# Kernel optimization log

Measured on AMD Instinct MI355X. Metric: run time of the kernel, lower is better.

## Reference

```python
import jax, jax.numpy as jnp
import numpy as np

B, T, E, H = 2, 2048, 1024, 4
Dk = E // H          # 256 head qk dim
Dv = Dk * 2          # 512 head v dim (expansion_ratio=2)
EPS = 1e-5
ROPE_BASE = 10000.0


def setup_inputs() -> dict:
    key = jax.random.key(0)
    ks = jax.random.split(key, 7)
    s = 0.02  # small init matching xavier gains in reset_parameters
    return {
        "x": jax.random.normal(ks[0], (B, T, E), jnp.float32),
        "Wq": jax.random.normal(ks[1], (E, E), jnp.float32) * s,
        "Wk": jax.random.normal(ks[2], (E, E), jnp.float32) * s,
        "Wv": jax.random.normal(ks[3], (E, 2 * E), jnp.float32) * s,
        "Wg": jax.random.normal(ks[4], (E, 2 * E), jnp.float32) * s,
        "Wo": jax.random.normal(ks[5], (2 * E, E), jnp.float32) * s,
        "gn_weight": jnp.ones((Dv,), jnp.float32),
    }


def _rotary(q, k):
    # q,k: [b, t, h, d]; non-interleaved (GPT-NeoX) rotary over the full head dim
    d = q.shape[-1]
    inv_freq = 1.0 / (ROPE_BASE ** (jnp.arange(0, d, 2, dtype=jnp.float32) / d))
    t = jnp.arange(q.shape[1], dtype=jnp.float32)
    freqs = jnp.einsum('t,f->tf', t, inv_freq)      # [t, d/2]
    cos = jnp.cos(freqs)[None, :, None, :]
    sin = jnp.sin(freqs)[None, :, None, :]

    def rot(x):
        x1, x2 = x[..., : d // 2], x[..., d // 2:]
        return jnp.concatenate([x1 * cos - x2 * sin, x2 * cos + x1 * sin], axis=-1)

    return rot(q), rot(k)


def reference(x, Wq, Wk, Wv, Wg, Wo, gn_weight):
    b, t, e = x.shape
    q = (x @ Wq).reshape(b, t, H, Dk)
    k = (x @ Wk).reshape(b, t, H, Dk)
    q, k = _rotary(q, k)
    q = q.transpose(0, 2, 1, 3) * (Dk ** -0.5)      # [b,h,t,dk], scale = head_qk_dim^-0.5
    k = k.transpose(0, 2, 1, 3)
    v = (x @ Wv).reshape(b, t, H, Dv).transpose(0, 2, 1, 3)  # [b,h,t,dv]

    # RetNet per-head decay: gamma_h = 1 - 2^-(5+h)
    gamma = 1.0 - jnp.exp2(-5.0 - jnp.arange(H, dtype=jnp.float32))
    ti = jnp.arange(t)
    n = ti[:, None] - ti[None, :]                   # t - s
    decay = jnp.where(
        n >= 0,
        gamma[:, None, None] ** jnp.maximum(n, 0).astype(jnp.float32),
        0.0,
    )                                               # [h,t,t] causal decayed mask

    scores = jnp.einsum('bhtd,bhsd->bhts', q, k) * decay[None]
    o = jnp.einsum('bhts,bhsd->bhtd', scores, v)    # [b,h,t,dv]
    o = o.transpose(0, 2, 1, 3)                     # [b,t,h,dv]

    # per-head RMSNorm (group_norm over head_v_dim)
    rms = jnp.sqrt(jnp.mean(o * o, axis=-1, keepdims=True) + EPS)
    o = o / rms * gn_weight

    # NOTE: the given source multiplies by raw g_proj(x) (gate_fn not applied in forward)
    g = x @ Wg                                      # [b,t,2E]
    return (o.reshape(b, t, H * Dv) * g) @ Wo       # [b,t,E]
```

## Files before the change

### kernel.cpp

```cpp
#include <hip/hip_runtime.h>
#include <hip/hip_bf16.h>

#define B_ 2
#define T_ 2048
#define E_ 1024
#define DK 256
#define DV 512
#define MROWS 4096
#define LDQKVG 6144
#define LDOG 2048

typedef __attribute__((ext_vector_type(8))) short short8;
typedef __attribute__((ext_vector_type(4))) float floatx4;

typedef __attribute__((address_space(3))) unsigned as3_u32;
typedef const __attribute__((address_space(1))) unsigned as1_u32;

static __device__ __forceinline__ void gld_lds16(const unsigned short* gsrc, unsigned short* ldst) {
  __builtin_amdgcn_global_load_lds((as1_u32*)gsrc, (as3_u32*)ldst, 16, 0, 0);
}

static __device__ __forceinline__ float bf2f(unsigned short u) {
  union { unsigned int i; float f; } x; x.i = ((unsigned int)u) << 16; return x.f;
}
static __device__ __forceinline__ unsigned short f2bf(float f) {
  __hip_bfloat16 h = __float2bfloat16(f);
  return __builtin_bit_cast(unsigned short, h);
}
static __device__ __forceinline__ float load_as_f(const float* p) { return *p; }
static __device__ __forceinline__ float load_as_f(const unsigned short* p) { return bf2f(*p); }

__global__ void __launch_bounds__(256) convx_kernel(const float* __restrict__ x,
                                                    unsigned short* __restrict__ xb) {
  int i = blockIdx.x * 256 + threadIdx.x;
  size_t base = (size_t)i * 8;
  float4 a = *(const float4*)(x + base);
  float4 b = *(const float4*)(x + base + 4);
  short8 o;
  o[0] = (short)f2bf(a.x); o[1] = (short)f2bf(a.y);
  o[2] = (short)f2bf(a.z); o[3] = (short)f2bf(a.w);
  o[4] = (short)f2bf(b.x); o[5] = (short)f2bf(b.y);
  o[6] = (short)f2bf(b.z); o[7] = (short)f2bf(b.w);
  *(short8*)(xb + base) = o;
}

template<typename TIN>
__global__ void __launch_bounds__(256) transpose_bf16_kernel(
    const TIN* __restrict__ in, int ldin, unsigned short* __restrict__ out, int ldout) {
  __shared__ float tile[32][33];
  int c0 = blockIdx.x * 32, r0 = blockIdx.y * 32;
  int tx = threadIdx.x & 31, ty = threadIdx.x >> 5;
#pragma unroll
  for (int i = 0; i < 32; i += 8)
    tile[ty + i][tx] = load_as_f(&in[(size_t)(r0 + ty + i) * ldin + c0 + tx]);
  __syncthreads();
#pragma unroll
  for (int i = 0; i < 32; i += 8)
    out[(size_t)(c0 + ty + i) * ldout + r0 + tx] = f2bf(tile[tx][ty + i]);
}

template<int MTILE, bool F32OUT>
__global__ void __launch_bounds__(256) gemm_bt_kernel(
    const unsigned short* __restrict__ A, const unsigned short* __restrict__ Bt,
    void* __restrict__ Cp, int K, int ldc, int ccol0) {
  __shared__ unsigned short As[MTILE * 32];
  __shared__ unsigned short Bs[128 * 32];
  constexpr int MB = MTILE / 32;
  constexpr int AJ = MTILE / 64;
  const int tid = threadIdx.x;
  const int lane = tid & 63;
  const int wid = tid >> 6;
  const int m0 = blockIdx.x * MTILE;
  const int n0 = blockIdx.y * 128;
  const int wr = (wid >> 1) * (MTILE / 2), wc = (wid & 1) * 64;
  floatx4 acc[MB][4];
#pragma unroll
  for (int i = 0; i < MB; i++)
#pragma unroll
    for (int j = 0; j < 4; j++)
      acc[i][j] = (floatx4){0.f, 0.f, 0.f, 0.f};

  for (int k0 = 0; k0 < K; k0 += 32) {
    __syncthreads();
#pragma unroll
    for (int j = 0; j < AJ; ++j) {
      int ci = (wid * AJ + j) * 64 + lane;
      int row = ci >> 2, cc = (ci & 3) * 8;
      gld_lds16(&A[(size_t)(m0 + row) * K + k0 + cc], &As[(wid * AJ + j) * 512]);
    }
#pragma unroll
    for (int j = 0; j < 2; ++j) {
      int ci = (wid * 2 + j) * 64 + lane;
      int row = ci >> 2, cc = (ci & 3) * 8;
      gld_lds16(&Bt[(size_t)(n0 + row) * K + k0 + cc], &Bs[(wid * 2 + j) * 512]);
    }
    __syncthreads();
    short8 af[MB], bfr[4];
#pragma unroll
    for (int mb = 0; mb < MB; mb++)
      af[mb] = *(const short8*)&As[(wr + mb * 16 + (lane & 15)) * 32 + (lane >> 4) * 8];
#pragma unroll
    for (int nb = 0; nb < 4; nb++)
      bfr[nb] = *(const short8*)&Bs[(wc + nb * 16 + (lane & 15)) * 32 + (lane >> 4) * 8];
#pragma unroll
    for (int mb = 0; mb < MB; mb++)
#pragma unroll
      for (int nb = 0; nb < 4; nb++)
        acc[mb][nb] = __builtin_amdgcn_mfma_f32_16x16x32_bf16(af[mb], bfr[nb], acc[mb][nb], 0, 0, 0);
  }
#pragma unroll
  for (int mb = 0; mb < MB; mb++)
#pragma unroll
    for (int nb = 0; nb < 4; nb++)
#pragma unroll
      for (int r = 0; r < 4; r++) {
        int row = m0 + wr + mb * 16 + (lane >> 4) * 4 + r;
        int col = ccol0 + n0 + wc + nb * 16 + (lane & 15);
        float v = acc[mb][nb][r];
        if (F32OUT) ((float*)Cp)[(size_t)row * ldc + col] = v;
        else ((unsigned short*)Cp)[(size_t)row * ldc + col] = f2bf(v);
      }
}

__global__ void __launch_bounds__(256) rope_kernel(unsigned short* __restrict__ qkvg) {
  int idx = blockIdx.x * 256 + threadIdx.x;
  int j = idx & 127;
  int h = (idx >> 7) & 3;
  int row = idx >> 9;
  int t = row & (T_ - 1);
  float invf = exp2f(-(float)j * (13.287712379549449f / 128.0f));
  float ang = (float)t * invf;
  float c = cosf(ang), s = sinf(ang);
  size_t base = (size_t)row * LDQKVG + h * DK + j;
  float q1 = bf2f(qkvg[base]), q2 = bf2f(qkvg[base + 128]);
  float k1 = bf2f(qkvg[base + E_]), k2 = bf2f(qkvg[base + E_ + 128]);
  qkvg[base]            = f2bf((q1 * c - q2 * s) * 0.0625f);
  qkvg[base + 128]      = f2bf((q2 * c + q1 * s) * 0.0625f);
  qkvg[base + E_]       = f2bf(k1 * c - k2 * s);
  qkvg[base + E_ + 128] = f2bf(k2 * c + k1 * s);
}

__global__ void __launch_bounds__(256) retention_kernel(
    const unsigned short* __restrict__ qkvg, const unsigned short* __restrict__ vT,
    const float* __restrict__ gnw, unsigned short* __restrict__ og,
    float* __restrict__ ssbuf) {
  __shared__ unsigned short k_lds[2][32 * 256];
  __shared__ unsigned short v_lds[2][256 * 32];
  __shared__ unsigned short s_lds[2][16 * 40];
  __shared__ float rms_lds[32][2];
  const int tid = threadIdx.x, lane = tid & 63, wid = tid >> 6;
  const int rh = wid & 1, dh = wid >> 1;
  const int bh = blockIdx.x & 7, dvh = (blockIdx.x >> 3) & 1, p = blockIdx.x >> 4;
  const int b = bh >> 2, h = bh & 3;
  const float log2g = log2f(1.0f - exp2f(-5.0f - (float)h));
  const unsigned short* kbase = qkvg + (size_t)b * T_ * LDQKVG + E_ + h * DK;
  const unsigned short* vbase = vT + (size_t)(h * DV + dvh * 256) * MROWS + b * T_;

  auto stage = [&](int buf, int sb) {
    int s0 = sb * 32;
#pragma unroll
    for (int j = 0; j < 4; ++j) {
      int ci = (wid * 4 + j) * 64 + lane;
      int row = ci >> 5, c = ci & 31;
      int cs = c ^ (row & 7);
      gld_lds16(kbase + (size_t)(s0 + row) * LDQKVG + cs * 8, &k_lds[buf][(wid * 4 + j) * 512]);
    }
#pragma unroll
    for (int j = 0; j < 4; ++j) {
      int ci = (wid * 4 + j) * 64 + lane;
      int dv = ci >> 2, c = ci & 3;
      int cs = c ^ ((dv ^ (dv >> 2)) & 3);
      gld_lds16(vbase + (size_t)dv * MROWS + s0 + cs * 8, &v_lds[buf][(wid * 4 + j) * 512]);
    }
  };

#pragma unroll 1
  for (int half = 0; half < 2; ++half) {
    const int tt = half == 0 ? p : 63 - p;
    const int r0 = tt * 32;
    const int nsb = tt + 1;

    short8 qf[8];
    {
      int qrow = b * T_ + r0 + rh * 16 + (lane & 15);
      const unsigned short* qp = qkvg + (size_t)qrow * LDQKVG + h * DK + (lane >> 4) * 8;
#pragma unroll
      for (int kk = 0; kk < 8; kk++) qf[kk] = *(const short8*)(qp + kk * 32);
    }
    floatx4 oacc[8];
#pragma unroll
    for (int i = 0; i < 8; i++) oacc[i] = (floatx4){0.f, 0.f, 0.f, 0.f};

    stage(0, 0);
#pragma unroll 1
    for (int sb = 0; sb < nsb; ++sb) {
      const int cur = sb & 1;
      __syncthreads();
      floatx4 f = (floatx4){0.f, 0.f, 0.f, 0.f};
      const int scol_l = dh * 16 + (lane & 15);
#pragma unroll
      for (int kk = 0; kk < 8; kk++) {
        int c = (kk * 4 + (lane >> 4)) ^ (scol_l & 7);
        short8 kf = *(const short8*)&k_lds[cur][scol_l * 256 + c * 8];
        f = __builtin_amdgcn_mfma_f32_16x16x32_bf16(qf[kk], kf, f, 0, 0, 0);
      }
      const int s0 = sb * 32;
#pragma unroll
      for (int r = 0; r < 4; ++r) {
        int lr = (lane >> 4) * 4 + r;
        int qrow_h = r0 + rh * 16 + lr;
        int scol = s0 + dh * 16 + (lane & 15);
        int n = qrow_h - scol;
        float val = (n >= 0) ? f[r] * exp2f((float)n * log2g) : 0.0f;
        s_lds[rh][lr * 40 + dh * 16 + (lane & 15)] = f2bf(val);
      }
      __syncthreads();
      if (sb + 1 < nsb) stage(cur ^ 1, sb + 1);
      short8 af = *(const short8*)&s_lds[rh][(lane & 15) * 40 + (lane >> 4) * 8];
#pragma unroll
      for (int nb = 0; nb < 8; ++nb) {
        int dv = dh * 128 + nb * 16 + (lane & 15);
        int c = (lane >> 4) ^ ((dv ^ (dv >> 2)) & 3);
        short8 vf = *(const short8*)&v_lds[cur][dv * 32 + c * 8];
        oacc[nb] = __builtin_amdgcn_mfma_f32_16x16x32_bf16(af, vf, oacc[nb], 0, 0, 0);
      }
    }
#pragma unroll
    for (int r = 0; r < 4; ++r) {
      float ss = 0.f;
#pragma unroll
      for (int nb = 0; nb < 8; nb++) { float xv = oacc[nb][r]; ss += xv * xv; }
      ss += __shfl_xor(ss, 1, 64);
      ss += __shfl_xor(ss, 2, 64);
      ss += __shfl_xor(ss, 4, 64);
      ss += __shfl_xor(ss, 8, 64);
      if ((lane & 15) == 0) rms_lds[rh * 16 + (lane >> 4) * 4 + r][dh] = ss;
    }
    __syncthreads();
    if (dh == 0 && (lane & 15) == 0) {
#pragma unroll
      for (int r = 0; r < 4; ++r) {
        int rl = rh * 16 + (lane >> 4) * 4 + r;
        ssbuf[(size_t)(b * T_ + r0 + rl) * 8 + h * 2 + dvh] = rms_lds[rl][0] + rms_lds[rl][1];
      }
    }
#pragma unroll
    for (int r = 0; r < 4; ++r) {
      int rl = rh * 16 + (lane >> 4) * 4 + r;
      int qrow = b * T_ + r0 + rl;
      size_t growbase = (size_t)qrow * LDQKVG + 4096 + h * DV + dvh * 256 + dh * 128;
      size_t orowbase = (size_t)qrow * LDOG + h * DV + dvh * 256 + dh * 128;
#pragma unroll
      for (int nb = 0; nb < 8; nb++) {
        int col = nb * 16 + (lane & 15);
        float gv = bf2f(qkvg[growbase + col]);
        og[orowbase + col] = f2bf(oacc[nb][r] * gnw[dvh * 256 + dh * 128 + col] * gv);
      }
    }
    __syncthreads();
  }
}

__global__ void __launch_bounds__(256) normalize_kernel(
    unsigned short* __restrict__ og, const float* __restrict__ ssbuf) {
  int i = blockIdx.x * 256 + threadIdx.x;
  size_t e0 = (size_t)i * 8;
  int row = (int)(e0 >> 11);
  int col = (int)(e0 & 2047);
  int h = col >> 9;
  float ss = ssbuf[(size_t)row * 8 + h * 2] + ssbuf[(size_t)row * 8 + h * 2 + 1];
  float inv = rsqrtf(ss * (1.0f / 512.0f) + 1e-5f);
  short8 v = *(const short8*)(og + e0);
#pragma unroll
  for (int j = 0; j < 8; j++) v[j] = (short)f2bf(bf2f((unsigned short)v[j]) * inv);
  *(short8*)(og + e0) = v;
}

extern "C" void kernel_launch(void* const* d_in, const int* in_sizes, int n_in,
                              void* d_out, int out_size, void* d_ws, size_t ws_size,
                              hipStream_t stream) {
  const float* x   = (const float*)d_in[0];
  const float* Wq  = (const float*)d_in[1];
  const float* Wk  = (const float*)d_in[2];
  const float* Wv  = (const float*)d_in[3];
  const float* Wg  = (const float*)d_in[4];
  const float* Wo  = (const float*)d_in[5];
  const float* gnw = (const float*)d_in[6];
  float* out = (float*)d_out;

  char* ws = (char*)d_ws;
  size_t off = 0;
  auto alloc = [&](size_t bytes) { char* p = ws + off; off += (bytes + 255) & ~(size_t)255; return p; };
  unsigned short* xb    = (unsigned short*)alloc((size_t)MROWS * E_ * 2);
  unsigned short* WallT = (unsigned short*)alloc((size_t)6144 * 1024 * 2);
  unsigned short* WoT   = (unsigned short*)alloc((size_t)1024 * 2048 * 2);
  unsigned short* qkvg  = (unsigned short*)alloc((size_t)MROWS * LDQKVG * 2);
  unsigned short* vT    = (unsigned short*)alloc((size_t)2048 * MROWS * 2);
  unsigned short* og    = (unsigned short*)alloc((size_t)MROWS * LDOG * 2);
  float*          ssbuf = (float*)alloc((size_t)MROWS * 8 * 4);

  convx_kernel<<<2048, 256, 0, stream>>>(x, xb);

  transpose_bf16_kernel<float><<<dim3(32, 32), 256, 0, stream>>>(Wq, 1024, WallT, 1024);
  transpose_bf16_kernel<float><<<dim3(32, 32), 256, 0, stream>>>(Wk, 1024, WallT + (size_t)1024 * 1024, 1024);
  transpose_bf16_kernel<float><<<dim3(64, 32), 256, 0, stream>>>(Wv, 2048, WallT + (size_t)2048 * 1024, 1024);
  transpose_bf16_kernel<float><<<dim3(64, 32), 256, 0, stream>>>(Wg, 2048, WallT + (size_t)4096 * 1024, 1024);
  transpose_bf16_kernel<float><<<dim3(32, 64), 256, 0, stream>>>(Wo, 1024, WoT, 2048);

  gemm_bt_kernel<128, false><<<dim3(32, 48), 256, 0, stream>>>(xb, WallT, qkvg, 1024, LDQKVG, 0);

  rope_kernel<<<8192, 256, 0, stream>>>(qkvg);

  transpose_bf16_kernel<unsigned short><<<dim3(64, 128), 256, 0, stream>>>(qkvg + 2048, LDQKVG, vT, MROWS);

  retention_kernel<<<512, 256, 0, stream>>>(qkvg, vT, gnw, og, ssbuf);

  normalize_kernel<<<4096, 256, 0, stream>>>(og, ssbuf);

  gemm_bt_kernel<64, true><<<dim3(64, 8), 256, 0, stream>>>(og, WoT, out, 2048, E_, 0);
}
```

Before: 240.7 us.

## Switch retention to chunkwise form with inter-chunk recurrent state

```diff
diff --git a/kernel.cpp b/kernel.cpp
--- a/kernel.cpp
+++ b/kernel.cpp
@@ -8,9 +8,11 @@
 #define DV 512
 #define MROWS 4096
 #define LDQKVG 6144
-#define LDOG 2048
+#define CHK 128
+#define NCHK 16
 
 typedef __attribute__((ext_vector_type(8))) short short8;
+typedef __attribute__((ext_vector_type(4))) short short4v;
 typedef __attribute__((ext_vector_type(4))) float floatx4;
 
 typedef __attribute__((address_space(3))) unsigned as3_u32;
@@ -59,10 +61,29 @@
     out[(size_t)(c0 + ty + i) * ldout + r0 + tx] = f2bf(tile[tx][ty + i]);
 }
 
+__global__ void __launch_bounds__(256) kts_transpose_kernel(
+    const unsigned short* __restrict__ in, unsigned short* __restrict__ out) {
+  __shared__ float tile[32][33];
+  int c0 = blockIdx.x * 32, r0 = blockIdx.y * 32;
+  int tx = threadIdx.x & 31, ty = threadIdx.x >> 5;
+#pragma unroll
+  for (int i = 0; i < 32; i += 8)
+    tile[ty + i][tx] = bf2f(in[(size_t)(r0 + ty + i) * LDQKVG + c0 + tx]);
+  __syncthreads();
+  int h = c0 >> 8;
+  float lg = log2f(1.0f - exp2f(-5.0f - (float)h));
+  int t = r0 + tx;
+  float fac = exp2f((float)(CHK - (t & (CHK - 1))) * lg);
+#pragma unroll
+  for (int i = 0; i < 32; i += 8)
+    out[(size_t)(c0 + ty + i) * MROWS + r0 + tx] = f2bf(tile[tx][ty + i] * fac);
+}
+
 template<int MTILE, bool F32OUT>
-__global__ void __launch_bounds__(256) gemm_bt_kernel(
-    const unsigned short* __restrict__ A, const unsigned short* __restrict__ Bt,
-    void* __restrict__ Cp, int K, int ldc, int ccol0) {
+static __device__ __forceinline__ void gemm_tile(
+    const unsigned short* __restrict__ A, int lda,
+    const unsigned short* __restrict__ Bt, int ldb,
+    int K, char* __restrict__ Cbase, int ldc) {
   __shared__ unsigned short As[MTILE * 32];
   __shared__ unsigned short Bs[128 * 32];
   constexpr int MB = MTILE / 32;
@@ -70,8 +91,6 @@
   const int tid = threadIdx.x;
   const int lane = tid & 63;
   const int wid = tid >> 6;
-  const int m0 = blockIdx.x * MTILE;
-  const int n0 = blockIdx.y * 128;
   const int wr = (wid >> 1) * (MTILE / 2), wc = (wid & 1) * 64;
   floatx4 acc[MB][4];
 #pragma unroll
@@ -86,13 +105,13 @@
     for (int j = 0; j < AJ; ++j) {
       int ci = (wid * AJ + j) * 64 + lane;
       int row = ci >> 2, cc = (ci & 3) * 8;
-      gld_lds16(&A[(size_t)(m0 + row) * K + k0 + cc], &As[(wid * AJ + j) * 512]);
+      gld_lds16(&A[(size_t)row * lda + k0 + cc], &As[(wid * AJ + j) * 512]);
     }
 #pragma unroll
     for (int j = 0; j < 2; ++j) {
       int ci = (wid * 2 + j) * 64 + lane;
       int row = ci >> 2, cc = (ci & 3) * 8;
-      gld_lds16(&Bt[(size_t)(n0 + row) * K + k0 + cc], &Bs[(wid * 2 + j) * 512]);
+      gld_lds16(&Bt[(size_t)row * ldb + k0 + cc], &Bs[(wid * 2 + j) * 512]);
     }
     __syncthreads();
     short8 af[MB], bfr[4];
@@ -114,12 +133,24 @@
     for (int nb = 0; nb < 4; nb++)
 #pragma unroll
       for (int r = 0; r < 4; r++) {
-        int row = m0 + wr + mb * 16 + (lane >> 4) * 4 + r;
-        int col = ccol0 + n0 + wc + nb * 16 + (lane & 15);
+        int row = wr + mb * 16 + (lane >> 4) * 4 + r;
+        int col = wc + nb * 16 + (lane & 15);
         float v = acc[mb][nb][r];
-        if (F32OUT) ((float*)Cp)[(size_t)row * ldc + col] = v;
-        else ((unsigned short*)Cp)[(size_t)row * ldc + col] = f2bf(v);
+        if (F32OUT) ((float*)Cbase)[(size_t)row * ldc + col] = v;
+        else ((unsigned short*)Cbase)[(size_t)row * ldc + col] = f2bf(v);
       }
+}
+
+template<int MTILE, bool F32OUT>
+__global__ void __launch_bounds__(256) gemm_bt_kernel(
+    const unsigned short* __restrict__ A, int lda,
+    const unsigned short* __restrict__ Bt, int ldb, int K,
+    void* __restrict__ Cp, int ldc, int ccol0) {
+  size_t m0 = (size_t)blockIdx.x * MTILE;
+  size_t n0 = (size_t)blockIdx.y * 128;
+  size_t esz = F32OUT ? 4 : 2;
+  gemm_tile<MTILE, F32OUT>(A + m0 * lda, lda, Bt + n0 * ldb, ldb, K,
+                           (char*)Cp + esz * (m0 * ldc + ccol0 + n0), ldc);
 }
 
 __global__ void __launch_bounds__(256) rope_kernel(unsigned short* __restrict__ qkvg) {
@@ -131,133 +162,176 @@
   float invf = exp2f(-(float)j * (13.287712379549449f / 128.0f));
   float ang = (float)t * invf;
   float c = cosf(ang), s = sinf(ang);
+  float lg = log2f(1.0f - exp2f(-5.0f - (float)h));
+  float sq = 0.0625f * exp2f((float)(t & (CHK - 1)) * lg);
   size_t base = (size_t)row * LDQKVG + h * DK + j;
   float q1 = bf2f(qkvg[base]), q2 = bf2f(qkvg[base + 128]);
   float k1 = bf2f(qkvg[base + E_]), k2 = bf2f(qkvg[base + E_ + 128]);
-  qkvg[base]            = f2bf((q1 * c - q2 * s) * 0.0625f);
-  qkvg[base + 128]      = f2bf((q2 * c + q1 * s) * 0.0625f);
+  qkvg[base]            = f2bf((q1 * c - q2 * s) * sq);
+  qkvg[base + 128]      = f2bf((q2 * c + q1 * s) * sq);
   qkvg[base + E_]       = f2bf(k1 * c - k2 * s);
   qkvg[base + E_ + 128] = f2bf(k2 * c + k1 * s);
 }
 
-__global__ void __launch_bounds__(256) retention_kernel(
+__global__ void __launch_bounds__(256) state_kernel(
+    const unsigned short* __restrict__ kTs, const unsigned short* __restrict__ vT,
+    unsigned short* __restrict__ Sbuf) {
+  const int lane = threadIdx.x & 63, wid = threadIdx.x >> 6;
+  const int bh = blockIdx.x & 7, dkt = (blockIdx.x >> 3) & 3, dvt = (blockIdx.x >> 5) & 15;
+  const int b = bh >> 2, h = bh & 3;
+  const float lg = log2f(1.0f - exp2f(-5.0f - (float)h));
+  const float g128 = exp2f((float)CHK * lg);
+  const int dk0 = dkt * 64 + wid * 16;
+  const int dv0 = dvt * 32;
+  const unsigned short* arow = kTs + (size_t)(h * DK + dk0 + (lane & 15)) * MROWS + b * T_ + (lane >> 4) * 8;
+  const unsigned short* brow = vT + (size_t)(h * DV + dv0 + (lane & 15)) * MROWS + b * T_ + (lane >> 4) * 8;
+  floatx4 acc[2];
+  acc[0] = (floatx4){0.f, 0.f, 0.f, 0.f};
+  acc[1] = (floatx4){0.f, 0.f, 0.f, 0.f};
+#pragma unroll 1
+  for (int c = 0; c < NCHK; ++c) {
+    size_t sb = (size_t)(c * 8 + bh) * (DV * DK);
+#pragma unroll
+    for (int nb = 0; nb < 2; ++nb) {
+      short4v o;
+#pragma unroll
+      for (int r = 0; r < 4; ++r) o[r] = (short)f2bf(acc[nb][r]);
+      *(short4v*)&Sbuf[sb + (size_t)(dv0 + nb * 16 + (lane & 15)) * DK + dk0 + (lane >> 4) * 4] = o;
+    }
+#pragma unroll
+    for (int nb = 0; nb < 2; ++nb)
+#pragma unroll
+      for (int r = 0; r < 4; ++r) acc[nb][r] *= g128;
+#pragma unroll
+    for (int ks = 0; ks < 4; ++ks) {
+      short8 a = *(const short8*)(arow + c * CHK + ks * 32);
+#pragma unroll
+      for (int nb = 0; nb < 2; ++nb) {
+        short8 bb = *(const short8*)(brow + (size_t)nb * 16 * MROWS + c * CHK + ks * 32);
+        acc[nb] = __builtin_amdgcn_mfma_f32_16x16x32_bf16(a, bb, acc[nb], 0, 0, 0);
+      }
+    }
+  }
+}
+
+__global__ void __launch_bounds__(256) retention2_kernel(
     const unsigned short* __restrict__ qkvg, const unsigned short* __restrict__ vT,
-    const float* __restrict__ gnw, unsigned short* __restrict__ og,
-    float* __restrict__ ssbuf) {
+    const unsigned short* __restrict__ Sbuf, const float* __restrict__ gnw,
+    unsigned short* __restrict__ og, float* __restrict__ ssbuf) {
   __shared__ unsigned short k_lds[2][32 * 256];
   __shared__ unsigned short v_lds[2][256 * 32];
-  __shared__ unsigned short s_lds[2][16 * 40];
-  __shared__ float rms_lds[32][2];
+  __shared__ unsigned short s_lds[4][16 * 40];
   const int tid = threadIdx.x, lane = tid & 63, wid = tid >> 6;
-  const int rh = wid & 1, dh = wid >> 1;
-  const int bh = blockIdx.x & 7, dvh = (blockIdx.x >> 3) & 1, p = blockIdx.x >> 4;
+  const int bh  = blockIdx.x & 7;
+  const int c   = (blockIdx.x >> 3) & 15;
+  const int dvh = (blockIdx.x >> 7) & 1;
+  const int rhf = (blockIdx.x >> 8) & 1;
   const int b = bh >> 2, h = bh & 3;
-  const float log2g = log2f(1.0f - exp2f(-5.0f - (float)h));
-  const unsigned short* kbase = qkvg + (size_t)b * T_ * LDQKVG + E_ + h * DK;
-  const unsigned short* vbase = vT + (size_t)(h * DV + dvh * 256) * MROWS + b * T_;
-
-  auto stage = [&](int buf, int sb) {
-    int s0 = sb * 32;
+  const float lg = log2f(1.0f - exp2f(-5.0f - (float)h));
+  const int rb0 = b * T_ + c * CHK + rhf * 64;
+  const int taub = rhf * 64 + wid * 16;
+  const int nst = rhf ? 4 : 2;
+  const unsigned short* kbase = qkvg + (size_t)(b * T_ + c * CHK) * LDQKVG + E_ + h * DK;
+  const unsigned short* vbase = vT + (size_t)(h * DV + dvh * 256) * MROWS + b * T_ + c * CHK;
+  const unsigned short* Sp = Sbuf + (size_t)(c * 8 + bh) * (DV * DK) + (size_t)dvh * 256 * DK;
+
+  auto stage = [&](int buf, int st) {
+    int s0 = st * 32;
 #pragma unroll
     for (int j = 0; j < 4; ++j) {
       int ci = (wid * 4 + j) * 64 + lane;
-      int row = ci >> 5, c = ci & 31;
-      int cs = c ^ (row & 7);
+      int row = ci >> 5, cc = ci & 31;
+      int cs = cc ^ (row & 7);
       gld_lds16(kbase + (size_t)(s0 + row) * LDQKVG + cs * 8, &k_lds[buf][(wid * 4 + j) * 512]);
     }
 #pragma unroll
     for (int j = 0; j < 4; ++j) {
       int ci = (wid * 4 + j) * 64 + lane;
-      int dv = ci >> 2, c = ci & 3;
-      int cs = c ^ ((dv ^ (dv >> 2)) & 3);
+      int dv = ci >> 2, cc = ci & 3;
+      int cs = cc ^ ((dv ^ (dv >> 2)) & 3);
       gld_lds16(vbase + (size_t)dv * MROWS + s0 + cs * 8, &v_lds[buf][(wid * 4 + j) * 512]);
     }
   };
 
+  stage(0, 0);
+
+  short8 qf[8];
+  {
+    int qrow = rb0 + wid * 16 + (lane & 15);
+    const unsigned short* qp = qkvg + (size_t)qrow * LDQKVG + h * DK + (lane >> 4) * 8;
+#pragma unroll
+    for (int kk = 0; kk < 8; kk++) qf[kk] = *(const short8*)(qp + kk * 32);
+  }
+  floatx4 oacc[16];
+#pragma unroll
+  for (int nb = 0; nb < 16; ++nb) oacc[nb] = (floatx4){0.f, 0.f, 0.f, 0.f};
+#pragma unroll
+  for (int ks = 0; ks < 8; ++ks) {
+#pragma unroll
+    for (int nb = 0; nb < 16; ++nb) {
+      short8 sf = *(const short8*)&Sp[(size_t)(nb * 16 + (lane & 15)) * DK + ks * 32 + (lane >> 4) * 8];
+      oacc[nb] = __builtin_amdgcn_mfma_f32_16x16x32_bf16(qf[ks], sf, oacc[nb], 0, 0, 0);
+    }
+  }
+
 #pragma unroll 1
-  for (int half = 0; half < 2; ++half) {
-    const int tt = half == 0 ? p : 63 - p;
-    const int r0 = tt * 32;
-    const int nsb = tt + 1;
-
-    short8 qf[8];
-    {
-      int qrow = b * T_ + r0 + rh * 16 + (lane & 15);
-      const unsigned short* qp = qkvg + (size_t)qrow * LDQKVG + h * DK + (lane >> 4) * 8;
-#pragma unroll
-      for (int kk = 0; kk < 8; kk++) qf[kk] = *(const short8*)(qp + kk * 32);
-    }
-    floatx4 oacc[8];
-#pragma unroll
-    for (int i = 0; i < 8; i++) oacc[i] = (floatx4){0.f, 0.f, 0.f, 0.f};
-
-    stage(0, 0);
-#pragma unroll 1
-    for (int sb = 0; sb < nsb; ++sb) {
-      const int cur = sb & 1;
-      __syncthreads();
+  for (int st = 0; st < nst; ++st) {
+    const int cur = st & 1;
+    __syncthreads();
+    if (st + 1 < nst) stage(cur ^ 1, st + 1);
+#pragma unroll
+    for (int ch = 0; ch < 2; ++ch) {
       floatx4 f = (floatx4){0.f, 0.f, 0.f, 0.f};
-      const int scol_l = dh * 16 + (lane & 15);
+      const int srow = ch * 16 + (lane & 15);
 #pragma unroll
       for (int kk = 0; kk < 8; kk++) {
-        int c = (kk * 4 + (lane >> 4)) ^ (scol_l & 7);
-        short8 kf = *(const short8*)&k_lds[cur][scol_l * 256 + c * 8];
+        int cc = (kk * 4 + (lane >> 4)) ^ (srow & 7);
+        short8 kf = *(const short8*)&k_lds[cur][srow * 256 + cc * 8];
         f = __builtin_amdgcn_mfma_f32_16x16x32_bf16(qf[kk], kf, f, 0, 0, 0);
       }
-      const int s0 = sb * 32;
 #pragma unroll
       for (int r = 0; r < 4; ++r) {
         int lr = (lane >> 4) * 4 + r;
-        int qrow_h = r0 + rh * 16 + lr;
-        int scol = s0 + dh * 16 + (lane & 15);
-        int n = qrow_h - scol;
-        float val = (n >= 0) ? f[r] * exp2f((float)n * log2g) : 0.0f;
-        s_lds[rh][lr * 40 + dh * 16 + (lane & 15)] = f2bf(val);
+        int sig = st * 32 + ch * 16 + (lane & 15);
+        int n = taub + lr - sig;
+        float val = (n >= 0) ? f[r] * exp2f(-(float)sig * lg) : 0.0f;
+        s_lds[wid][lr * 40 + ch * 16 + (lane & 15)] = f2bf(val);
       }
-      __syncthreads();
-      if (sb + 1 < nsb) stage(cur ^ 1, sb + 1);
-      short8 af = *(const short8*)&s_lds[rh][(lane & 15) * 40 + (lane >> 4) * 8];
-#pragma unroll
-      for (int nb = 0; nb < 8; ++nb) {
-        int dv = dh * 128 + nb * 16 + (lane & 15);
-        int c = (lane >> 4) ^ ((dv ^ (dv >> 2)) & 3);
-        short8 vf = *(const short8*)&v_lds[cur][dv * 32 + c * 8];
-        oacc[nb] = __builtin_amdgcn_mfma_f32_16x16x32_bf16(af, vf, oacc[nb], 0, 0, 0);
-      }
-    }
-#pragma unroll
-    for (int r = 0; r < 4; ++r) {
-      float ss = 0.f;
-#pragma unroll
-      for (int nb = 0; nb < 8; nb++) { float xv = oacc[nb][r]; ss += xv * xv; }
-      ss += __shfl_xor(ss, 1, 64);
-      ss += __shfl_xor(ss, 2, 64);
-      ss += __shfl_xor(ss, 4, 64);
-      ss += __shfl_xor(ss, 8, 64);
-      if ((lane & 15) == 0) rms_lds[rh * 16 + (lane >> 4) * 4 + r][dh] = ss;
-    }
-    __syncthreads();
-    if (dh == 0 && (lane & 15) == 0) {
-#pragma unroll
-      for (int r = 0; r < 4; ++r) {
-        int rl = rh * 16 + (lane >> 4) * 4 + r;
-        ssbuf[(size_t)(b * T_ + r0 + rl) * 8 + h * 2 + dvh] = rms_lds[rl][0] + rms_lds[rl][1];
-      }
-    }
-#pragma unroll
-    for (int r = 0; r < 4; ++r) {
-      int rl = rh * 16 + (lane >> 4) * 4 + r;
-      int qrow = b * T_ + r0 + rl;
-      size_t growbase = (size_t)qrow * LDQKVG + 4096 + h * DV + dvh * 256 + dh * 128;
-      size_t orowbase = (size_t)qrow * LDOG + h * DV + dvh * 256 + dh * 128;
-#pragma unroll
-      for (int nb = 0; nb < 8; nb++) {
-        int col = nb * 16 + (lane & 15);
-        float gv = bf2f(qkvg[growbase + col]);
-        og[orowbase + col] = f2bf(oacc[nb][r] * gnw[dvh * 256 + dh * 128 + col] * gv);
-      }
-    }
-    __syncthreads();
+    }
+    short8 af = *(const short8*)&s_lds[wid][(lane & 15) * 40 + (lane >> 4) * 8];
+#pragma unroll
+    for (int nb = 0; nb < 16; ++nb) {
+      int dv = nb * 16 + (lane & 15);
+      int cc = (lane >> 4) ^ ((dv ^ (dv >> 2)) & 3);
+      short8 vf = *(const short8*)&v_lds[cur][dv * 32 + cc * 8];
+      oacc[nb] = __builtin_amdgcn_mfma_f32_16x16x32_bf16(af, vf, oacc[nb], 0, 0, 0);
+    }
+  }
+#pragma unroll
+  for (int r = 0; r < 4; ++r) {
+    float ss = 0.f;
+#pragma unroll
+    for (int nb = 0; nb < 16; nb++) { float xv = oacc[nb][r]; ss += xv * xv; }
+    ss += __shfl_xor(ss, 1, 64);
+    ss += __shfl_xor(ss, 2, 64);
+    ss += __shfl_xor(ss, 4, 64);
+    ss += __shfl_xor(ss, 8, 64);
+    if ((lane & 15) == 0) {
+      int row = rb0 + wid * 16 + (lane >> 4) * 4 + r;
+      ssbuf[(size_t)row * 8 + h * 2 + dvh] = ss;
+    }
+  }
+#pragma unroll
+  for (int r = 0; r < 4; ++r) {
+    int row = rb0 + wid * 16 + (lane >> 4) * 4 + r;
+    size_t growbase = (size_t)row * LDQKVG + 4096 + h * DV + dvh * 256;
+    size_t orowbase = (size_t)row * LDQKVG + h * DV + dvh * 256;
+#pragma unroll
+    for (int nb = 0; nb < 16; nb++) {
+      int col = nb * 16 + (lane & 15);
+      float gv = bf2f(qkvg[growbase + col]);
+      og[orowbase + col] = f2bf(oacc[nb][r] * gnw[dvh * 256 + col] * gv);
+    }
   }
 }
 
@@ -270,10 +344,11 @@
   int h = col >> 9;
   float ss = ssbuf[(size_t)row * 8 + h * 2] + ssbuf[(size_t)row * 8 + h * 2 + 1];
   float inv = rsqrtf(ss * (1.0f / 512.0f) + 1e-5f);
-  short8 v = *(const short8*)(og + e0);
+  size_t a = (size_t)row * LDQKVG + col;
+  short8 v = *(const short8*)(og + a);
 #pragma unroll
   for (int j = 0; j < 8; j++) v[j] = (short)f2bf(bf2f((unsigned short)v[j]) * inv);
-  *(short8*)(og + e0) = v;
+  *(short8*)(og + a) = v;
 }
 
 extern "C" void kernel_launch(void* const* d_in, const int* in_sizes, int n_in,
@@ -291,13 +366,17 @@
   char* ws = (char*)d_ws;
   size_t off = 0;
   auto alloc = [&](size_t bytes) { char* p = ws + off; off += (bytes + 255) & ~(size_t)255; return p; };
-  unsigned short* xb    = (unsigned short*)alloc((size_t)MROWS * E_ * 2);
-  unsigned short* WallT = (unsigned short*)alloc((size_t)6144 * 1024 * 2);
-  unsigned short* WoT   = (unsigned short*)alloc((size_t)1024 * 2048 * 2);
-  unsigned short* qkvg  = (unsigned short*)alloc((size_t)MROWS * LDQKVG * 2);
-  unsigned short* vT    = (unsigned short*)alloc((size_t)2048 * MROWS * 2);
-  unsigned short* og    = (unsigned short*)alloc((size_t)MROWS * LDOG * 2);
-  float*          ssbuf = (float*)alloc((size_t)MROWS * 8 * 4);
+  unsigned short* qkvg = (unsigned short*)alloc((size_t)MROWS * LDQKVG * 2);
+  unsigned short* vT   = (unsigned short*)alloc((size_t)2048 * MROWS * 2);
+  char* regS = alloc((size_t)NCHK * 8 * DV * DK * 2);
+  unsigned short* Sbuf  = (unsigned short*)regS;
+  unsigned short* xb    = (unsigned short*)regS;
+  unsigned short* WallT = (unsigned short*)(regS + 8388608);
+  char* regK = alloc((size_t)1024 * MROWS * 2);
+  unsigned short* kTs = (unsigned short*)regK;
+  unsigned short* WoT = (unsigned short*)regK;
+  float* ssbuf = (float*)alloc((size_t)MROWS * 8 * 4);
+  unsigned short* og = qkvg + 2048;
 
   convx_kernel<<<2048, 256, 0, stream>>>(x, xb);
 
@@ -305,17 +384,22 @@
   transpose_bf16_kernel<float><<<dim3(32, 32), 256, 0, stream>>>(Wk, 1024, WallT + (size_t)1024 * 1024, 1024);
   transpose_bf16_kernel<float><<<dim3(64, 32), 256, 0, stream>>>(Wv, 2048, WallT + (size_t)2048 * 1024, 1024);
   transpose_bf16_kernel<float><<<dim3(64, 32), 256, 0, stream>>>(Wg, 2048, WallT + (size_t)4096 * 1024, 1024);
+
+  gemm_bt_kernel<128, false><<<dim3(32, 48), 256, 0, stream>>>(xb, 1024, WallT, 1024, 1024, qkvg, LDQKVG, 0);
+
+  rope_kernel<<<8192, 256, 0, stream>>>(qkvg);
+
+  kts_transpose_kernel<<<dim3(32, 128), 256, 0, stream>>>(qkvg + E_, kTs);
+
+  transpose_bf16_kernel<unsigned short><<<dim3(64, 128), 256, 0, stream>>>(qkvg + 2048, LDQKVG, vT, MROWS);
+
+  state_kernel<<<512, 256, 0, stream>>>(kTs, vT, Sbuf);
+
   transpose_bf16_kernel<float><<<dim3(32, 64), 256, 0, stream>>>(Wo, 1024, WoT, 2048);
 
-  gemm_bt_kernel<128, false><<<dim3(32, 48), 256, 0, stream>>>(xb, WallT, qkvg, 1024, LDQKVG, 0);
-
-  rope_kernel<<<8192, 256, 0, stream>>>(qkvg);
-
-  transpose_bf16_kernel<unsigned short><<<dim3(64, 128), 256, 0, stream>>>(qkvg + 2048, LDQKVG, vT, MROWS);
-
-  retention_kernel<<<512, 256, 0, stream>>>(qkvg, vT, gnw, og, ssbuf);
+  retention2_kernel<<<512, 256, 0, stream>>>(qkvg, vT, Sbuf, gnw, og, ssbuf);
 
   normalize_kernel<<<4096, 256, 0, stream>>>(og, ssbuf);
 
-  gemm_bt_kernel<64, true><<<dim3(64, 8), 256, 0, stream>>>(og, WoT, out, 2048, E_, 0);
-}
+  gemm_bt_kernel<64, true><<<dim3(64, 8), 256, 0, stream>>>(og, LDQKVG, WoT, 2048, 2048, out, E_, 0);
+}
```

Result: slower. 253.0 us (+5.1%).
